# Kernel tuning notes

Measured on AMD Instinct MI355X. Metric: run time of the kernel, lower is better.

## Reference

```python
import jax, jax.numpy as jnp
import numpy as np

N_HEADS = 4


def _mha(q, k, v, in_w, in_b, out_w, out_b):
    # torch nn.MultiheadAttention (batch_first). q: [..., Lq, C], k/v: [..., Lk, C].
    # Leading batch dims broadcast (used for the factorized per-slice attention).
    C = q.shape[-1]
    dh = C // N_HEADS
    wq, wk, wv = jnp.split(in_w, 3, axis=0)
    bq, bk, bv = jnp.split(in_b, 3, axis=0)
    qh = (q @ wq.T + bq).reshape(q.shape[:-1] + (N_HEADS, dh))
    kh = (k @ wk.T + bk).reshape(k.shape[:-1] + (N_HEADS, dh))
    vh = (v @ wv.T + bv).reshape(v.shape[:-1] + (N_HEADS, dh))
    logits = jnp.einsum('...qhd,...khd->...hqk', qh, kh) / np.sqrt(dh).astype(np.float32)
    alpha = jax.nn.softmax(logits, axis=-1)
    o = jnp.einsum('...hqk,...khd->...qhd', alpha, vh)
    o = o.reshape(o.shape[:-2] + (C,))
    return o @ out_w.T + out_b


def _layernorm(x, w, b):
    m = x.mean(-1, keepdims=True)
    v = x.var(-1, keepdims=True)
    return (x - m) * jax.lax.rsqrt(v + 1e-5) * w + b


def reference(h, hist0, hist1, dw_w, pw_w, gn_w, gn_b, gr1_scale, gr1_gw, gr1_gb,
              global_tokens, mha_in_w, mha_in_b, mha_out_w, mha_out_b,
              ln_w, ln_b, gr2_scale, gr2_gw, gr2_gb, rms_w, blk_w, Hx, Hy, Hz):
    B, N, C = h.shape
    M = global_tokens.shape[0]

    # ---------------- DepthwiseConv3d block ----------------
    # 'b (hz hy hx) c -> b c hx hy hz'
    h3 = h.reshape(B, Hz, Hy, Hx, C).transpose(0, 4, 3, 2, 1)  # [B,C,Hx,Hy,Hz]
    y = jax.lax.conv_general_dilated(
        h3, dw_w, window_strides=(1, 1, 1), padding=((1, 1), (1, 1), (1, 1)),
        dimension_numbers=('NCDHW', 'OIDHW', 'NCDHW'), feature_group_count=C)
    # GroupNorm(num_groups=min(32,C))
    G = min(32, C)
    yg = y.reshape(B, G, C // G, Hx, Hy, Hz)
    mu = yg.mean(axis=(2, 3, 4, 5), keepdims=True)
    var = yg.var(axis=(2, 3, 4, 5), keepdims=True)
    y = ((yg - mu) * jax.lax.rsqrt(var + 1e-5)).reshape(B, C, Hx, Hy, Hz)
    y = y * gn_w[None, :, None, None, None] + gn_b[None, :, None, None, None]
    y = jax.nn.gelu(y, approximate=False)  # torch nn.GELU default = exact erf
    y = jnp.einsum('bcxyz,oc->boxyz', y, pw_w)  # 1x1x1 pointwise conv
    delta = y.transpose(0, 4, 3, 2, 1).reshape(B, N, C)  # back to 'b (hz hy hx) c'
    h = h + gr1_scale * jax.nn.sigmoid(h @ gr1_gw.T + gr1_gb) * delta

    # ---------------- FactorizedCrossAttn ----------------
    h_xyz = h.reshape(B, Hz, Hy, Hx, C).transpose(0, 3, 2, 1, 4)  # [B,Hx,Hy,Hz,C]
    Q = jnp.broadcast_to(global_tokens, (B, M, C))
    Qb = Q[:, None]  # [B,1,M,C]; broadcasts over slices instead of materializing expand

    kv_x = h_xyz.transpose(0, 2, 3, 1, 4).reshape(B, Hy * Hz, Hx, C)
    tok_x = _mha(Qb, kv_x, kv_x, mha_in_w[0], mha_in_b[0], mha_out_w[0], mha_out_b[0]).mean(1)
    kv_y = h_xyz.transpose(0, 1, 3, 2, 4).reshape(B, Hx * Hz, Hy, C)
    tok_y = _mha(Qb, kv_y, kv_y, mha_in_w[1], mha_in_b[1], mha_out_w[1], mha_out_b[1]).mean(1)
    kv_z = h_xyz.reshape(B, Hx * Hy, Hz, C)
    tok_z = _mha(Qb, kv_z, kv_z, mha_in_w[2], mha_in_b[2], mha_out_w[2], mha_out_b[2]).mean(1)

    tokens = tok_x + tok_y + tok_z
    t_in = _layernorm(tokens, ln_w[0], ln_b[0])
    tokens = _mha(t_in, t_in, t_in, mha_in_w[3], mha_in_b[3], mha_out_w[3], mha_out_b[3])
    h_normed = _layernorm(h, ln_w[1], ln_b[1])
    glob = _mha(h_normed, tokens, tokens, mha_in_w[4], mha_in_b[4], mha_out_w[4], mha_out_b[4])
    h = h + gr2_scale * jax.nn.sigmoid(h @ gr2_gw.T + gr2_gb) * glob

    # ---------------- block_attn_res ----------------
    V = jnp.stack([hist0, hist1, h], axis=0)  # [S,B,N,C], S=3
    K = V * jax.lax.rsqrt(jnp.mean(V * V, axis=-1, keepdims=True) + 1e-6) * rms_w  # RMSNorm
    logits = jnp.clip(jnp.einsum('d,sbnd->sbn', blk_w, K), -30.0, 30.0)
    alpha = jax.nn.softmax(logits, axis=0)
    return jnp.einsum('sbn,sbnd->bnd', alpha, V)


def setup_inputs() -> dict:
    key = jax.random.key(0)
    ks = jax.random.split(key, 16)
    B, C, Hx, Hy, Hz, M = 2, 128, 64, 64, 32, 64
    N = Hx * Hy * Hz

    def g(k, shape, scale):
        return jax.random.normal(k, shape, dtype=jnp.float32) * scale

    return {
        'h': g(ks[0], (B, N, C), 1.0),
        'hist0': g(ks[1], (B, N, C), 1.0),
        'hist1': g(ks[2], (B, N, C), 1.0),
        'dw_w': g(ks[3], (C, 1, 3, 3, 3), 0.27),  # kaiming_normal_ fan_in=27
        'pw_w': jnp.ones((C, C), jnp.float32) / C,  # code uses ones_; scaled for stability
        'gn_w': jnp.ones((C,), jnp.float32),
        'gn_b': jnp.zeros((C,), jnp.float32),
        'gr1_scale': jnp.float32(0.01),
        'gr1_gw': g(ks[4], (C, C), 0.02),
        'gr1_gb': jnp.zeros((C,), jnp.float32),
        'global_tokens': g(ks[5], (M, C), 0.09),  # xavier_uniform-ish scale
        'mha_in_w': g(ks[6], (5, 3 * C, C), 0.06),
        'mha_in_b': jnp.zeros((5, 3 * C), jnp.float32),
        'mha_out_w': g(ks[7], (5, C, C), 0.06),
        'mha_out_b': jnp.zeros((5, C), jnp.float32),
        'ln_w': jnp.ones((2, C), jnp.float32),
        'ln_b': jnp.zeros((2, C), jnp.float32),
        'gr2_scale': jnp.float32(0.01),
        'gr2_gw': g(ks[8], (C, C), 0.02),
        'gr2_gb': jnp.zeros((C,), jnp.float32),
        'rms_w': jnp.ones((C,), jnp.float32),
        'blk_w': g(ks[9], (C,), 0.09),
        'Hx': Hx, 'Hy': Hy, 'Hz': Hz,
    }
```

## Files before the change

kernel.cpp:

```cpp
#include <hip/hip_runtime.h>
#include <hip/hip_bf16.h>

#define B_ 2
#define C_ 128
#define HX_ 64
#define HY_ 64
#define HZ_ 32
#define N_ 131072
#define M_ 64
#define G_ 32
#define SCALE_ 0.17677669529663687f

typedef unsigned short u16;
typedef __bf16 bf16x8 __attribute__((ext_vector_type(8)));
typedef float f32x4 __attribute__((ext_vector_type(4)));

#define MFMA(a, b, c) __builtin_amdgcn_mfma_f32_16x16x32_bf16(a, b, c, 0, 0, 0)

__device__ __forceinline__ float bf2f(u16 u){
    return __uint_as_float(((unsigned int)u) << 16);
}
__device__ __forceinline__ u16 f2bf(float f){
    unsigned int u = __float_as_uint(f);
    unsigned int r = (u + 0x7FFFu + ((u >> 16) & 1u)) >> 16;
    return (u16)r;
}
__device__ __forceinline__ bf16x8 ldf(const u16* p){
    return __builtin_bit_cast(bf16x8, *reinterpret_cast<const uint4*>(p));
}
__device__ __forceinline__ float wred_sum(float v){
    for (int o = 32; o; o >>= 1) v += __shfl_xor(v, o);
    return v;
}

__global__ __launch_bounds__(256) void k_wcvt(const float* __restrict__ pw, const float* __restrict__ g1w,
        const float* __restrict__ in_w, const float* __restrict__ out_w, const float* __restrict__ g2w,
        u16* __restrict__ wA, u16* __restrict__ wKV, u16* __restrict__ wQ, u16* __restrict__ wO, u16* __restrict__ wG2){
    int idx = blockIdx.x*256 + threadIdx.x;
    if (idx < 32768){
        int j = idx >> 7, k = idx & 127;
        wA[idx] = f2bf(j < 128 ? pw[j*128 + k] : g1w[(j-128)*128 + k]);
    } else if (idx < 131072){
        int r = idx - 32768;
        int a = r >> 15, jk = r & 32767;
        int j = jk >> 7, k = jk & 127;
        wKV[r] = f2bf(in_w[((size_t)a*384 + 128 + j)*128 + k]);
    } else if (idx < 147456){
        int r = idx - 131072;
        wQ[r] = f2bf(in_w[4*384*128 + r]);
    } else if (idx < 163840){
        int r = idx - 147456;
        wO[r] = f2bf(out_w[4*128*128 + r]);
    } else if (idx < 180224){
        int r = idx - 163840;
        wG2[r] = f2bf(g2w[r]);
    }
}

__global__ __launch_bounds__(256, 2) void k_conv3(const float* __restrict__ h,
        const float* __restrict__ dw_w, u16* __restrict__ ybf, u16* __restrict__ hb16,
        float* __restrict__ gstats){
    int t = threadIdx.x;
    int lane = t & 31;
    int c4 = lane << 2;
    int xg = t >> 5;
    int bi = blockIdx.x;
    int b = bi >> 9;
    int y = (bi >> 3) & 63;
    int x = ((bi & 7) << 3) | xg;
    const float* hb = h + (size_t)b*N_*C_;
    u16* yb = ybf + (size_t)b*N_*C_;
    u16* hbb = hb16 + (size_t)b*N_*C_;
    f32x4 wv[27];
    int off[9];
    #pragma unroll
    for (int dxi = 0; dxi < 3; ++dxi){
        #pragma unroll
        for (int dyi = 0; dyi < 3; ++dyi){
            int xr = x + dxi - 1, yr = y + dyi - 1;
            float m = (xr >= 0 && xr < HX_ && yr >= 0 && yr < HY_) ? 1.f : 0.f;
            int xx = min(max(xr, 0), HX_-1);
            int yy = min(max(yr, 0), HY_-1);
            off[dxi*3+dyi] = (yy*64 + xx)*128 + c4;
            #pragma unroll
            for (int dzi = 0; dzi < 3; ++dzi){
                int k = (dxi*3+dyi)*3+dzi;
                int wk = dxi*9 + dyi*3 + dzi;
                f32x4 wq;
                #pragma unroll
                for (int e = 0; e < 4; ++e) wq[e] = dw_w[(c4+e)*27 + wk] * m;
                wv[k] = wq;
            }
        }
    }
    f32x4 accA = {0,0,0,0}, accB = {0,0,0,0}, accC = {0,0,0,0};
    f32x4 sum4 = {0,0,0,0}, ss4 = {0,0,0,0};
    #pragma unroll 2
    for (int zp = 0; zp < 32; ++zp){
        size_t zb = (size_t)zp*524288;
        f32x4 v[9];
        #pragma unroll
        for (int j = 0; j < 9; ++j) v[j] = *(const f32x4*)(hb + zb + off[j]);
        {
            unsigned int p0 = (unsigned int)f2bf(v[4][0]) | ((unsigned int)f2bf(v[4][1]) << 16);
            unsigned int p1 = (unsigned int)f2bf(v[4][2]) | ((unsigned int)f2bf(v[4][3]) << 16);
            uint2 pk = {p0, p1};
            *(uint2*)(hbb + zb + off[4]) = pk;
        }
        f32x4 s0 = {0,0,0,0}, s1 = {0,0,0,0}, s2 = {0,0,0,0};
        #pragma unroll
        for (int j = 0; j < 9; ++j){
            s0 += v[j]*wv[j*3+0];
            s1 += v[j]*wv[j*3+1];
            s2 += v[j]*wv[j*3+2];
        }
        accA += s2; accB += s1; accC += s0;
        if (zp >= 1){
            f32x4 yv = accA;
            sum4 += yv; ss4 += yv*yv;
            unsigned int p0 = (unsigned int)f2bf(yv[0]) | ((unsigned int)f2bf(yv[1]) << 16);
            unsigned int p1 = (unsigned int)f2bf(yv[2]) | ((unsigned int)f2bf(yv[3]) << 16);
            uint2 pk = {p0, p1};
            *(uint2*)(yb + (size_t)(zp-1)*524288 + off[4]) = pk;
        }
        accA = accB; accB = accC; accC = (f32x4){0,0,0,0};
    }
    {
        f32x4 yv = accA;
        sum4 += yv; ss4 += yv*yv;
        unsigned int p0 = (unsigned int)f2bf(yv[0]) | ((unsigned int)f2bf(yv[1]) << 16);
        unsigned int p1 = (unsigned int)f2bf(yv[2]) | ((unsigned int)f2bf(yv[3]) << 16);
        uint2 pk = {p0, p1};
        *(uint2*)(yb + (size_t)31*524288 + off[4]) = pk;
    }
    float sum = sum4[0]+sum4[1]+sum4[2]+sum4[3];
    float ss  = ss4[0]+ss4[1]+ss4[2]+ss4[3];
    sum += __shfl_xor(sum, 32);
    ss  += __shfl_xor(ss, 32);
    if ((t & 32) == 0){
        atomicAdd(&gstats[(b*G_ + lane)*2 + 0], sum);
        atomicAdd(&gstats[(b*G_ + lane)*2 + 1], ss);
    }
}

__global__ void k_gstats_fin(const float* __restrict__ gstats, float* __restrict__ gfin){
    int t = threadIdx.x;
    if (t < B_*G_){
        const float cnt = 4.f * (float)N_;
        float mean = gstats[t*2] / cnt;
        float var  = gstats[t*2+1] / cnt - mean*mean;
        gfin[t*2]   = mean;
        gfin[t*2+1] = rsqrtf(var + 1e-5f);
    }
}

__global__ __launch_bounds__(256) void k_stageA(const u16* __restrict__ ybf, const u16* __restrict__ hb16,
        const float* __restrict__ gfin, const float* __restrict__ gn_w, const float* __restrict__ gn_b,
        const float* __restrict__ g1b, const float* __restrict__ s1p,
        const u16* __restrict__ wA, u16* __restrict__ h1b){
    __shared__ __align__(16) u16 sU[64*136];
    __shared__ __align__(16) u16 sH[64*136];
    __shared__ float sPar[384];
    int t = threadIdx.x;
    int w = t >> 6, l = t & 63, lm = l & 15, kq = l >> 4;
    if (t < 128){ sPar[t] = gn_w[t]; sPar[128+t] = gn_b[t]; sPar[256+t] = gfin[t]; }
    bf16x8 wUf[2][4], wGf[2][4];
    float gbias[2];
    #pragma unroll
    for (int jt = 0; jt < 2; ++jt){
        int j = w*32 + jt*16 + lm;
        gbias[jt] = g1b[j];
        #pragma unroll
        for (int ks = 0; ks < 4; ++ks){
            wUf[jt][ks] = ldf(wA + (size_t)j*128 + ks*32 + kq*8);
            wGf[jt][ks] = ldf(wA + (size_t)(128+j)*128 + ks*32 + kq*8);
        }
    }
    float s1 = s1p[0];
    __syncthreads();
    for (int it = 0; it < 4; ++it){
        int tile = blockIdx.x + it*1024;
        size_t r0 = (size_t)tile*64;
        int bsel = (tile >= 2048) ? 1 : 0;
        for (int pass = 0; pass < 4; ++pass){
            int cid = pass*256 + t;
            int row = cid >> 4, col8 = (cid & 15)*8;
            size_t gi = (r0 + row)*C_ + col8;
            uint4 yraw = *(const uint4*)(ybf + gi);
            uint4 hraw = *(const uint4*)(hb16 + gi);
            const u16* yp = (const u16*)&yraw;
            unsigned int pu[4];
            #pragma unroll
            for (int p2 = 0; p2 < 4; ++p2){
                u16 r2[2];
                #pragma unroll
                for (int e2 = 0; e2 < 2; ++e2){
                    int e = p2*2 + e2;
                    int ch = col8 + e;
                    int g = ch >> 2;
                    float mean = sPar[256 + (bsel*32+g)*2];
                    float inv  = sPar[256 + (bsel*32+g)*2 + 1];
                    float v = (bf2f(yp[e]) - mean)*inv*sPar[ch] + sPar[128+ch];
                    float u = 0.5f*v*(1.f + erff(v*0.70710678118654752f));
                    r2[e2] = f2bf(u);
                }
                pu[p2] = (unsigned int)r2[0] | ((unsigned int)r2[1] << 16);
            }
            *(uint4*)(sU + row*136 + col8) = *(uint4*)pu;
            *(uint4*)(sH + row*136 + col8) = hraw;
        }
        __syncthreads();
        f32x4 accU[4][2], accG[4][2];
        #pragma unroll
        for (int rt = 0; rt < 4; ++rt)
            #pragma unroll
            for (int jt = 0; jt < 2; ++jt){
                accU[rt][jt] = (f32x4){0.f,0.f,0.f,0.f};
                accG[rt][jt] = (f32x4){gbias[jt],gbias[jt],gbias[jt],gbias[jt]};
            }
        #pragma unroll
        for (int rt = 0; rt < 4; ++rt)
            #pragma unroll
            for (int ks = 0; ks < 4; ++ks){
                bf16x8 aU = ldf(sU + (rt*16+lm)*136 + ks*32 + kq*8);
                bf16x8 aH = ldf(sH + (rt*16+lm)*136 + ks*32 + kq*8);
                #pragma unroll
                for (int jt = 0; jt < 2; ++jt){
                    accU[rt][jt] = MFMA(aU, wUf[jt][ks], accU[rt][jt]);
                    accG[rt][jt] = MFMA(aH, wGf[jt][ks], accG[rt][jt]);
                }
            }
        #pragma unroll
        for (int rt = 0; rt < 4; ++rt)
            #pragma unroll
            for (int jt = 0; jt < 2; ++jt){
                int col = w*32 + jt*16 + lm;
                #pragma unroll
                for (int r = 0; r < 4; ++r){
                    int lrow = rt*16 + kq*4 + r;
                    float g = 1.f/(1.f + expf(-accG[rt][jt][r]));
                    float hv = bf2f(sH[lrow*136 + col]);
                    float h1v = hv + s1*g*accU[rt][jt][r];
                    h1b[(r0 + lrow)*C_ + col] = f2bf(h1v);
                }
            }
        __syncthreads();
    }
}

__global__ __launch_bounds__(256) void k_qh_axes(const float* __restrict__ gtok,
        const float* __restrict__ in_w, const float* __restrict__ in_b, float* __restrict__ qhT){
    int idx = blockIdx.x*256 + threadIdx.x;
    int m = idx & 63;
    int hd = (idx >> 6) & 127;
    int a = idx >> 13;
    float acc = in_b[a*384 + hd];
    const float* w = in_w + ((size_t)a*384 + hd)*C_;
    const float* q = gtok + (size_t)m*C_;
    for (int c = 0; c < C_; ++c) acc += q[c]*w[c];
    qhT[idx] = acc;
}

template<int AXIS, int L, int S>
__global__ __launch_bounds__(256, 2) void k_axis_attn(const u16* __restrict__ h1b,
        const u16* __restrict__ wKVb, const float* __restrict__ in_b,
        const float* __restrict__ qhT, float* __restrict__ o_mean){
    constexpr int SLICES = 8;
    constexpr int PARTS = S / SLICES;
    constexpr int PSROW = L + 8;
    constexpr int PSZ = 64 * PSROW;
    constexpr int NT = L / 16;
    constexpr int KS = L / 32;
    __shared__ __align__(16) u16 sm[6*PSZ];
    int t = threadIdx.x;
    int w = t >> 6, l = t & 63, lm = l & 15, kq = l >> 4;
    int b = blockIdx.x / PARTS;
    int part = blockIdx.x % PARTS;
    u16* rows = sm;
    u16* kv   = sm + 2*PSZ;
    u16* vT   = sm + 4*PSZ;
    u16* Ps   = sm + w*PSZ;
    bf16x8 wf[4][4];
    float bias[4];
    #pragma unroll
    for (int jt = 0; jt < 4; ++jt){
        int j = w*64 + jt*16 + lm;
        bias[jt] = in_b[AXIS*384 + 128 + j];
        #pragma unroll
        for (int ks = 0; ks < 4; ++ks)
            wf[jt][ks] = ldf(wKVb + ((size_t)AXIS*256 + j)*128 + ks*32 + kq*8);
    }
    bf16x8 qf[4];
    #pragma unroll
    for (int mt = 0; mt < 4; ++mt){
        union { u16 u[8]; bf16x8 v; } tmp;
        #pragma unroll
        for (int e = 0; e < 8; ++e)
            tmp.u[e] = f2bf(qhT[(AXIS*C_ + w*32 + kq*8 + e)*64 + mt*16 + lm] * SCALE_);
        qf[mt] = tmp.v;
    }
    f32x4 oacc[4][2];
    #pragma unroll
    for (int mt = 0; mt < 4; ++mt)
        #pragma unroll
        for (int dt = 0; dt < 2; ++dt)
            oacc[mt][dt] = (f32x4){0.f,0.f,0.f,0.f};
    const u16* hb = h1b + (size_t)b*N_*C_;
    for (int si = 0; si < SLICES; ++si){
        int s = part*SLICES + si;
        for (int ci = t; ci < L*16; ci += 256){
            int p = ci >> 4, c8 = (ci & 15)*8;
            int n;
            if (AXIS == 0){ int yy = s >> 5, zz = s & 31; n = zz*4096 + yy*64 + p; }
            else if (AXIS == 1){ int xx = s >> 5, zz = s & 31; n = zz*4096 + p*64 + xx; }
            else { int xx = s >> 6, yy = s & 63; n = p*4096 + yy*64 + xx; }
            *(uint4*)(rows + p*136 + c8) = *(const uint4*)(hb + (size_t)n*C_ + c8);
        }
        __syncthreads();
        #pragma unroll
        for (int rt = 0; rt < NT; ++rt){
            f32x4 acc[4];
            #pragma unroll
            for (int jt = 0; jt < 4; ++jt) acc[jt] = (f32x4){bias[jt],bias[jt],bias[jt],bias[jt]};
            #pragma unroll
            for (int ks = 0; ks < 4; ++ks){
                bf16x8 a = ldf(rows + (rt*16+lm)*136 + ks*32 + kq*8);
                #pragma unroll
                for (int jt = 0; jt < 4; ++jt) acc[jt] = MFMA(a, wf[jt][ks], acc[jt]);
            }
            #pragma unroll
            for (int jt = 0; jt < 4; ++jt){
                int j = w*64 + jt*16 + lm;
                #pragma unroll
                for (int r = 0; r < 4; ++r){
                    int key = rt*16 + kq*4 + r;
                    if (w < 2) kv[key*136 + j] = f2bf(acc[jt][r]);
                    else       vT[(j-128)*PSROW + key] = f2bf(acc[jt][r]);
                }
            }
        }
        __syncthreads();
        f32x4 lacc[4][NT];
        #pragma unroll
        for (int mt = 0; mt < 4; ++mt)
            #pragma unroll
            for (int nt = 0; nt < NT; ++nt) lacc[mt][nt] = (f32x4){0.f,0.f,0.f,0.f};
        #pragma unroll
        for (int nt = 0; nt < NT; ++nt){
            bf16x8 kf = ldf(kv + (nt*16+lm)*136 + w*32 + kq*8);
            #pragma unroll
            for (int mt = 0; mt < 4; ++mt) lacc[mt][nt] = MFMA(qf[mt], kf, lacc[mt][nt]);
        }
        __syncthreads();
        #pragma unroll
        for (int mt = 0; mt < 4; ++mt){
            #pragma unroll
            for (int r = 0; r < 4; ++r){
                float mx = lacc[mt][0][r];
                #pragma unroll
                for (int nt = 1; nt < NT; ++nt) mx = fmaxf(mx, lacc[mt][nt][r]);
                mx = fmaxf(mx, __shfl_xor(mx,1));
                mx = fmaxf(mx, __shfl_xor(mx,2));
                mx = fmaxf(mx, __shfl_xor(mx,4));
                mx = fmaxf(mx, __shfl_xor(mx,8));
                float ev[NT]; float sum = 0.f;
                #pragma unroll
                for (int nt = 0; nt < NT; ++nt){ ev[nt] = expf(lacc[mt][nt][r] - mx); sum += ev[nt]; }
                sum += __shfl_xor(sum,1);
                sum += __shfl_xor(sum,2);
                sum += __shfl_xor(sum,4);
                sum += __shfl_xor(sum,8);
                float inv = 1.f/sum;
                #pragma unroll
                for (int nt = 0; nt < NT; ++nt)
                    Ps[(mt*16 + kq*4 + r)*PSROW + nt*16 + lm] = f2bf(ev[nt]*inv);
            }
        }
        #pragma unroll
        for (int ks = 0; ks < KS; ++ks){
            bf16x8 vb[2];
            #pragma unroll
            for (int dt = 0; dt < 2; ++dt)
                vb[dt] = ldf(vT + (w*32 + dt*16 + lm)*PSROW + ks*32 + kq*8);
            #pragma unroll
            for (int mt = 0; mt < 4; ++mt){
                bf16x8 pa = ldf(Ps + (mt*16+lm)*PSROW + ks*32 + kq*8);
                #pragma unroll
                for (int dt = 0; dt < 2; ++dt)
                    oacc[mt][dt] = MFMA(pa, vb[dt], oacc[mt][dt]);
            }
        }
        __syncthreads();
    }
    const float invS = 1.f / (float)S;
    float* om = o_mean + (size_t)(AXIS*B_ + b)*M_*C_;
    #pragma unroll
    for (int mt = 0; mt < 4; ++mt)
        #pragma unroll
        for (int dt = 0; dt < 2; ++dt)
            #pragma unroll
            for (int r = 0; r < 4; ++r){
                int m = mt*16 + kq*4 + r;
                int d = dt*16 + lm;
                atomicAdd(&om[m*C_ + w*32 + d], oacc[mt][dt][r]*invS);
            }
}

__global__ __launch_bounds__(256) void k_tokens(const float* __restrict__ o_mean,
        const float* __restrict__ out_w, const float* __restrict__ out_b, float* __restrict__ tokens){
    int idx = blockIdx.x*256 + threadIdx.x;
    int c = idx & 127;
    int m = (idx >> 7) & 63;
    int b = idx >> 13;
    float acc = 0.f;
    for (int a = 0; a < 3; ++a){
        const float* om = o_mean + ((size_t)(a*B_ + b)*M_ + m)*C_;
        const float* w = out_w + ((size_t)a*C_ + c)*C_;
        float s = out_b[a*C_ + c];
        for (int k = 0; k < C_; ++k) s += om[k]*w[k];
        acc += s;
    }
    tokens[idx] = acc;
}

__global__ __launch_bounds__(128) void k_ln(const float* __restrict__ in,
        const float* __restrict__ w, const float* __restrict__ b, float* __restrict__ out){
    int r = blockIdx.x;
    int c = threadIdx.x;
    float v = in[(size_t)r*C_ + c];
    __shared__ float red[4];
    float s = wred_sum(v), ss = wred_sum(v*v);
    int wv = c >> 6;
    if ((c & 63) == 0){ red[wv*2] = s; red[wv*2+1] = ss; }
    __syncthreads();
    float S = red[0] + red[2], SS = red[1] + red[3];
    float mean = S / 128.f;
    float var = SS / 128.f - mean*mean;
    out[(size_t)r*C_ + c] = (v - mean) * rsqrtf(var + 1e-5f) * w[c] + b[c];
}

__global__ __launch_bounds__(256) void k_qkv3(const float* __restrict__ t_in,
        const float* __restrict__ in_w, const float* __restrict__ in_b, float* __restrict__ qkv3){
    int idx = blockIdx.x*256 + threadIdx.x;
    int j = idx % 384;
    int m = (idx / 384) & 63;
    int b = idx / (384*64);
    const float* x = t_in + ((size_t)b*64 + m)*C_;
    const float* w = in_w + ((size_t)3*384 + j)*C_;
    float acc = in_b[3*384 + j];
    for (int c = 0; c < C_; ++c) acc += x[c]*w[c];
    qkv3[idx] = acc;
}

__global__ __launch_bounds__(64) void k_attn3(const float* __restrict__ qkv3, float* __restrict__ o3){
    int b = blockIdx.x >> 2, hh = blockIdx.x & 3;
    int m = threadIdx.x;
    const float* base = qkv3 + (size_t)b*64*384;
    float q[32];
    #pragma unroll
    for (int d = 0; d < 32; ++d) q[d] = base[m*384 + hh*32 + d];
    float lg[64]; float mx = -1e30f;
    for (int mk = 0; mk < 64; ++mk){
        float acc = 0.f;
        #pragma unroll
        for (int d = 0; d < 32; ++d) acc += q[d] * base[mk*384 + 128 + hh*32 + d];
        acc *= SCALE_;
        lg[mk] = acc; mx = fmaxf(mx, acc);
    }
    float sum = 0.f;
    #pragma unroll
    for (int mk = 0; mk < 64; ++mk){ float e = expf(lg[mk]-mx); lg[mk] = e; sum += e; }
    float inv = 1.f/sum;
    float o[32];
    #pragma unroll
    for (int d = 0; d < 32; ++d) o[d] = 0.f;
    for (int mk = 0; mk < 64; ++mk){
        float al = lg[mk]*inv;
        #pragma unroll
        for (int d = 0; d < 32; ++d) o[d] += al * base[mk*384 + 256 + hh*32 + d];
    }
    #pragma unroll
    for (int d = 0; d < 32; ++d) o3[((size_t)b*64 + m)*C_ + hh*32 + d] = o[d];
}

__global__ __launch_bounds__(256) void k_tokens2(const float* __restrict__ o3,
        const float* __restrict__ out_w, const float* __restrict__ out_b, float* __restrict__ tokens2){
    int idx = blockIdx.x*256 + threadIdx.x;
    int c = idx & 127;
    int m = (idx >> 7) & 63;
    int b = idx >> 13;
    const float* x = o3 + ((size_t)b*64 + m)*C_;
    const float* w = out_w + ((size_t)3*C_ + c)*C_;
    float acc = out_b[3*C_ + c];
    for (int k = 0; k < C_; ++k) acc += x[k]*w[k];
    tokens2[idx] = acc;
}

__global__ __launch_bounds__(256) void k_kv4(const float* __restrict__ tokens2,
        const float* __restrict__ in_w, const float* __restrict__ in_b,
        u16* __restrict__ khs, u16* __restrict__ vhb){
    int idx = blockIdx.x*256 + threadIdx.x;
    int b = idx >> 14;
    int r = idx & 16383;
    if (r < 8192){
        int hh = r >> 11, key = (r >> 5) & 63, d = r & 31;
        int hd = hh*32 + d;
        const float* x = tokens2 + ((size_t)b*64 + key)*C_;
        const float* w = in_w + ((size_t)4*384 + 128 + hd)*C_;
        float acc = in_b[4*384 + 128 + hd];
        for (int c = 0; c < C_; ++c) acc += x[c]*w[c];
        khs[(size_t)b*8192 + r] = f2bf(acc * SCALE_);
    } else {
        int rr = r - 8192;
        int key = rr >> 7, c = rr & 127;
        const float* x = tokens2 + ((size_t)b*64 + key)*C_;
        const float* w = in_w + ((size_t)4*384 + 256 + c)*C_;
        float acc = in_b[4*384 + 256 + c];
        for (int k = 0; k < 128; ++k) acc += x[k]*w[k];
        vhb[(size_t)b*8192 + rr] = f2bf(acc);
    }
}

__global__ __launch_bounds__(256) void k_globfinal(const u16* __restrict__ h1b,
        const u16* __restrict__ wQb, const u16* __restrict__ wOb, const u16* __restrict__ wG2b,
        const u16* __restrict__ khs, const u16* __restrict__ vhb,
        const float* __restrict__ in_b, const float* __restrict__ out_b,
        const float* __restrict__ g2b, const float* __restrict__ s2p,
        const float* __restrict__ ln_w, const float* __restrict__ ln_b,
        const float* __restrict__ hist0, const float* __restrict__ hist1,
        const float* __restrict__ rms_w, const float* __restrict__ blk_w,
        float* __restrict__ outp){
    __shared__ __align__(16) u16 sm[22016];
    __shared__ float sLn[384];
    int t = threadIdx.x;
    int w = t >> 6, l = t & 63, lm = l & 15, kq = l >> 4;
    if (t < 128){ sLn[t] = ln_w[128+t]; sLn[128+t] = ln_b[128+t]; sLn[256+t] = blk_w[t]*rms_w[t]; }
    int b = blockIdx.x >> 9;
    bf16x8 wQf[2][4], wOf[2][4], wGf[2][4], khf[4], vf[2][2];
    float qb[2], ob[2], gb[2];
    #pragma unroll
    for (int jt = 0; jt < 2; ++jt){
        int j = w*32 + jt*16 + lm;
        qb[jt] = in_b[4*384 + j];
        ob[jt] = out_b[4*128 + j];
        gb[jt] = g2b[j];
        #pragma unroll
        for (int ks = 0; ks < 4; ++ks){
            wQf[jt][ks] = ldf(wQb + (size_t)j*128 + ks*32 + kq*8);
            wOf[jt][ks] = ldf(wOb + (size_t)j*128 + ks*32 + kq*8);
            wGf[jt][ks] = ldf(wG2b + (size_t)j*128 + ks*32 + kq*8);
        }
    }
    #pragma unroll
    for (int jt = 0; jt < 4; ++jt)
        khf[jt] = ldf(khs + ((size_t)(b*4 + w)*64 + jt*16 + lm)*32 + kq*8);
    #pragma unroll
    for (int jt = 0; jt < 2; ++jt)
        #pragma unroll
        for (int ks = 0; ks < 2; ++ks){
            union { u16 u[8]; bf16x8 v; } tmp;
            #pragma unroll
            for (int e = 0; e < 8; ++e){
                int key = ks*32 + kq*8 + e;
                tmp.u[e] = vhb[(size_t)(b*64 + key)*128 + w*32 + jt*16 + lm];
            }
            vf[jt][ks] = tmp.v;
        }
    float s2 = s2p[0];
    __syncthreads();

    for (int it = 0; it < 4; ++it){
        int tile = (blockIdx.x & 511) + it*512;
        size_t r0 = (size_t)b*N_ + (size_t)tile*64;
        {
            int r = t >> 2, q = t & 3;
            const u16* src = h1b + (r0 + r)*C_ + q*32;
            uint4 raw[4];
            float v[32];
            float s = 0.f, ss = 0.f;
            #pragma unroll
            for (int c4 = 0; c4 < 4; ++c4){
                raw[c4] = *(const uint4*)(src + c4*8);
                const u16* pu = (const u16*)&raw[c4];
                #pragma unroll
                for (int e = 0; e < 8; ++e){ float x = bf2f(pu[e]); v[c4*8+e] = x; s += x; ss += x*x; }
            }
            s += __shfl_xor(s,1); s += __shfl_xor(s,2);
            ss += __shfl_xor(ss,1); ss += __shfl_xor(ss,2);
            float mean = s*(1.f/128.f);
            float inv = rsqrtf(ss*(1.f/128.f) - mean*mean + 1e-5f);
            #pragma unroll
            for (int c4 = 0; c4 < 4; ++c4){
                unsigned int o[4];
                #pragma unroll
                for (int p2 = 0; p2 < 4; ++p2){
                    int c = q*32 + c4*8 + p2*2;
                    u16 a0 = f2bf((v[c4*8+p2*2]   - mean)*inv*sLn[c]   + sLn[128+c]);
                    u16 a1 = f2bf((v[c4*8+p2*2+1] - mean)*inv*sLn[c+1] + sLn[128+c+1]);
                    o[p2] = (unsigned int)a0 | ((unsigned int)a1 << 16);
                }
                *(uint4*)(sm + 0    + r*136 + q*32 + c4*8) = *(uint4*)o;
                *(uint4*)(sm + 8704 + r*136 + q*32 + c4*8) = raw[c4];
            }
        }
        __syncthreads();
        f32x4 accQ[4][2];
        #pragma unroll
        for (int rt = 0; rt < 4; ++rt)
            #pragma unroll
            for (int jt = 0; jt < 2; ++jt)
                accQ[rt][jt] = (f32x4){qb[jt],qb[jt],qb[jt],qb[jt]};
        #pragma unroll
        for (int rt = 0; rt < 4; ++rt)
            #pragma unroll
            for (int ks = 0; ks < 4; ++ks){
                bf16x8 a = ldf(sm + 0 + (rt*16+lm)*136 + ks*32 + kq*8);
                #pragma unroll
                for (int jt = 0; jt < 2; ++jt)
                    accQ[rt][jt] = MFMA(a, wQf[jt][ks], accQ[rt][jt]);
            }
        __syncthreads();
        #pragma unroll
        for (int rt = 0; rt < 4; ++rt)
            #pragma unroll
            for (int jt = 0; jt < 2; ++jt)
                #pragma unroll
                for (int r = 0; r < 4; ++r)
                    sm[0 + (rt*16+kq*4+r)*136 + w*32+jt*16+lm] = f2bf(accQ[rt][jt][r]);
        u16* Ps = sm + 17408 + w*1152;
        #pragma unroll
        for (int mt = 0; mt < 4; ++mt){
            bf16x8 aq = ldf(sm + 0 + (mt*16+lm)*136 + w*32 + kq*8);
            f32x4 lacc[4];
            #pragma unroll
            for (int jt = 0; jt < 4; ++jt) lacc[jt] = (f32x4){0.f,0.f,0.f,0.f};
            #pragma unroll
            for (int jt = 0; jt < 4; ++jt) lacc[jt] = MFMA(aq, khf[jt], lacc[jt]);
            #pragma unroll
            for (int r = 0; r < 4; ++r){
                float v0 = lacc[0][r], v1 = lacc[1][r], v2 = lacc[2][r], v3 = lacc[3][r];
                float mx = fmaxf(fmaxf(v0,v1), fmaxf(v2,v3));
                mx = fmaxf(mx, __shfl_xor(mx,1));
                mx = fmaxf(mx, __shfl_xor(mx,2));
                mx = fmaxf(mx, __shfl_xor(mx,4));
                mx = fmaxf(mx, __shfl_xor(mx,8));
                float e0 = expf(v0-mx), e1 = expf(v1-mx), e2 = expf(v2-mx), e3 = expf(v3-mx);
                float sum = e0+e1+e2+e3;
                sum += __shfl_xor(sum,1);
                sum += __shfl_xor(sum,2);
                sum += __shfl_xor(sum,4);
                sum += __shfl_xor(sum,8);
                float inv = 1.f/sum;
                Ps[(kq*4+r)*72 + lm     ] = f2bf(e0*inv);
                Ps[(kq*4+r)*72 + lm + 16] = f2bf(e1*inv);
                Ps[(kq*4+r)*72 + lm + 32] = f2bf(e2*inv);
                Ps[(kq*4+r)*72 + lm + 48] = f2bf(e3*inv);
            }
            f32x4 of[2];
            #pragma unroll
            for (int jt = 0; jt < 2; ++jt) of[jt] = (f32x4){0.f,0.f,0.f,0.f};
            #pragma unroll
            for (int ks = 0; ks < 2; ++ks){
                bf16x8 ap = ldf(Ps + lm*72 + ks*32 + kq*8);
                #pragma unroll
                for (int jt = 0; jt < 2; ++jt)
                    of[jt] = MFMA(ap, vf[jt][ks], of[jt]);
            }
            #pragma unroll
            for (int jt = 0; jt < 2; ++jt)
                #pragma unroll
                for (int r = 0; r < 4; ++r)
                    sm[0 + (mt*16+kq*4+r)*136 + w*32+jt*16+lm] = f2bf(of[jt][r]);
        }
        __syncthreads();
        f32x4 accO[4][2], accG[4][2];
        #pragma unroll
        for (int rt = 0; rt < 4; ++rt)
            #pragma unroll
            for (int jt = 0; jt < 2; ++jt){
                accO[rt][jt] = (f32x4){ob[jt],ob[jt],ob[jt],ob[jt]};
                accG[rt][jt] = (f32x4){gb[jt],gb[jt],gb[jt],gb[jt]};
            }
        #pragma unroll
        for (int rt = 0; rt < 4; ++rt)
            #pragma unroll
            for (int ks = 0; ks < 4; ++ks){
                bf16x8 ao = ldf(sm + 0    + (rt*16+lm)*136 + ks*32 + kq*8);
                bf16x8 ah = ldf(sm + 8704 + (rt*16+lm)*136 + ks*32 + kq*8);
                #pragma unroll
                for (int jt = 0; jt < 2; ++jt){
                    accO[rt][jt] = MFMA(ao, wOf[jt][ks], accO[rt][jt]);
                    accG[rt][jt] = MFMA(ah, wGf[jt][ks], accG[rt][jt]);
                }
            }
        #pragma unroll
        for (int rt = 0; rt < 4; ++rt)
            #pragma unroll
            for (int jt = 0; jt < 2; ++jt){
                int col = w*32 + jt*16 + lm;
                #pragma unroll
                for (int r = 0; r < 4; ++r){
                    int lrow = rt*16 + kq*4 + r;
                    float hv = bf2f(sm[8704 + lrow*136 + col]);
                    float g = 1.f/(1.f + expf(-accG[rt][jt][r]));
                    accO[rt][jt][r] = hv + s2*g*accO[rt][jt][r];
                }
            }
        __syncthreads();
        #pragma unroll
        for (int rt = 0; rt < 4; ++rt)
            #pragma unroll
            for (int jt = 0; jt < 2; ++jt){
                int col = w*32 + jt*16 + lm;
                #pragma unroll
                for (int r = 0; r < 4; ++r)
                    sm[8704 + (rt*16+kq*4+r)*132 + col] = f2bf(accO[rt][jt][r]);
            }
        __syncthreads();
        {
            int r = t >> 2, q = t & 3;
            size_t row = r0 + r;
            const u16* h2p = sm + 8704 + r*132 + q*32;
            float h2a[32], v0a[32], v1a[32];
            float ss0 = 0.f, ss1 = 0.f, ss2 = 0.f, q0 = 0.f, q1 = 0.f, q2 = 0.f;
            #pragma unroll
            for (int c4 = 0; c4 < 8; ++c4){
                uint2 hk = *(const uint2*)(h2p + c4*4);
                float4 a0 = *(const float4*)(hist0 + row*C_ + q*32 + c4*4);
                float4 a1 = *(const float4*)(hist1 + row*C_ + q*32 + c4*4);
                const u16* pu = (const u16*)&hk;
                const float* p0 = (const float*)&a0;
                const float* p1 = (const float*)&a1;
                #pragma unroll
                for (int e = 0; e < 4; ++e){
                    float bw = sLn[256 + q*32 + c4*4 + e];
                    float x2 = bf2f(pu[e]), x0 = p0[e], x1 = p1[e];
                    h2a[c4*4+e] = x2; v0a[c4*4+e] = x0; v1a[c4*4+e] = x1;
                    ss0 += x0*x0; ss1 += x1*x1; ss2 += x2*x2;
                    q0 += bw*x0; q1 += bw*x1; q2 += bw*x2;
                }
            }
            ss0 += __shfl_xor(ss0,1); ss0 += __shfl_xor(ss0,2);
            ss1 += __shfl_xor(ss1,1); ss1 += __shfl_xor(ss1,2);
            ss2 += __shfl_xor(ss2,1); ss2 += __shfl_xor(ss2,2);
            q0 += __shfl_xor(q0,1); q0 += __shfl_xor(q0,2);
            q1 += __shfl_xor(q1,1); q1 += __shfl_xor(q1,2);
            q2 += __shfl_xor(q2,1); q2 += __shfl_xor(q2,2);
            float i0 = rsqrtf(ss0*(1.f/128.f) + 1e-6f);
            float i1 = rsqrtf(ss1*(1.f/128.f) + 1e-6f);
            float i2 = rsqrtf(ss2*(1.f/128.f) + 1e-6f);
            float l0 = fminf(fmaxf(q0*i0, -30.f), 30.f);
            float l1 = fminf(fmaxf(q1*i1, -30.f), 30.f);
            float l2 = fminf(fmaxf(q2*i2, -30.f), 30.f);
            float mx = fmaxf(l0, fmaxf(l1, l2));
            float e0 = expf(l0-mx), e1 = expf(l1-mx), e2 = expf(l2-mx);
            float isum = 1.f/(e0+e1+e2);
            #pragma unroll
            for (int c4 = 0; c4 < 8; ++c4){
                float o[4];
                #pragma unroll
                for (int e = 0; e < 4; ++e){
                    int i = c4*4+e;
                    o[e] = (e0*v0a[i] + e1*v1a[i] + e2*h2a[i])*isum;
                }
                *(float4*)(outp + row*C_ + q*32 + c4*4) = *(float4*)o;
            }
        }
        __syncthreads();
    }
}

extern "C" void kernel_launch(void* const* d_in, const int* in_sizes, int n_in,
                              void* d_out, int out_size, void* d_ws, size_t ws_size,
                              hipStream_t stream){
    (void)in_sizes; (void)n_in; (void)out_size; (void)ws_size;
    const float* h     = (const float*)d_in[0];
    const float* hist0 = (const float*)d_in[1];
    const float* hist1 = (const float*)d_in[2];
    const float* dw_w  = (const float*)d_in[3];
    const float* pw_w  = (const float*)d_in[4];
    const float* gn_w  = (const float*)d_in[5];
    const float* gn_b  = (const float*)d_in[6];
    const float* gr1_s = (const float*)d_in[7];
    const float* gr1_gw= (const float*)d_in[8];
    const float* gr1_gb= (const float*)d_in[9];
    const float* gtok  = (const float*)d_in[10];
    const float* in_w  = (const float*)d_in[11];
    const float* in_b  = (const float*)d_in[12];
    const float* out_w = (const float*)d_in[13];
    const float* out_b = (const float*)d_in[14];
    const float* ln_w  = (const float*)d_in[15];
    const float* ln_b  = (const float*)d_in[16];
    const float* gr2_s = (const float*)d_in[17];
    const float* gr2_gw= (const float*)d_in[18];
    const float* gr2_gb= (const float*)d_in[19];
    const float* rms_w = (const float*)d_in[20];
    const float* blk_w = (const float*)d_in[21];
    float* out = (float*)d_out;

    u16* ybf  = (u16*)d_out;
    u16* hb16 = (u16*)d_out + (size_t)B_*N_*C_;

    float* W = (float*)d_ws;
    size_t off = 0;
    float* gstats  = W + off; off += 128;
    float* gfin    = W + off; off += 128;
    float* qhT     = W + off; off += 3*128*64;
    float* o_mean  = W + off; off += 3*B_*M_*C_;
    float* tokens  = W + off; off += B_*M_*C_;
    float* t_in    = W + off; off += B_*M_*C_;
    float* qkv3    = W + off; off += B_*M_*384;
    float* o3      = W + off; off += B_*M_*C_;
    float* tokens2 = W + off; off += B_*M_*C_;
    u16* U = (u16*)(W + off);
    size_t uo = 0;
    u16* h1b = U + uo; uo += (size_t)B_*N_*C_;
    u16* wA  = U + uo; uo += 256*128;
    u16* wKV = U + uo; uo += 3*256*128;
    u16* wQ  = U + uo; uo += 128*128;
    u16* wO  = U + uo; uo += 128*128;
    u16* wG2 = U + uo; uo += 128*128;
    u16* khs = U + uo; uo += B_*4*64*32;
    u16* vhb = U + uo; uo += B_*64*128;

    hipMemsetAsync(gstats, 0, 128*sizeof(float), stream);
    hipMemsetAsync(o_mean, 0, 3*B_*M_*C_*sizeof(float), stream);
    k_wcvt<<<704, 256, 0, stream>>>(pw_w, gr1_gw, in_w, out_w, gr2_gw, wA, wKV, wQ, wO, wG2);
    k_conv3<<<1024, 256, 0, stream>>>(h, dw_w, ybf, hb16, gstats);
    k_gstats_fin<<<1, 64, 0, stream>>>(gstats, gfin);
    k_stageA<<<1024, 256, 0, stream>>>(ybf, hb16, gfin, gn_w, gn_b, gr1_gb, gr1_s, wA, h1b);
    k_qh_axes<<<96, 256, 0, stream>>>(gtok, in_w, in_b, qhT);
    k_axis_attn<0,64,2048><<<512, 256, 0, stream>>>(h1b, wKV, in_b, qhT, o_mean);
    k_axis_attn<1,64,2048><<<512, 256, 0, stream>>>(h1b, wKV, in_b, qhT, o_mean);
    k_axis_attn<2,32,4096><<<1024, 256, 0, stream>>>(h1b, wKV, in_b, qhT, o_mean);
    k_tokens<<<64, 256, 0, stream>>>(o_mean, out_w, out_b, tokens);
    k_ln<<<B_*M_, 128, 0, stream>>>(tokens, ln_w, ln_b, t_in);
    k_qkv3<<<192, 256, 0, stream>>>(t_in, in_w, in_b, qkv3);
    k_attn3<<<8, 64, 0, stream>>>(qkv3, o3);
    k_tokens2<<<64, 256, 0, stream>>>(o3, out_w, out_b, tokens2);
    k_kv4<<<128, 256, 0, stream>>>(tokens2, in_w, in_b, khs, vhb);
    k_globfinal<<<1024, 256, 0, stream>>>(h1b, wQ, wO, wG2, khs, vhb, in_b, out_b,
                                          gr2_gb, gr2_s, ln_w, ln_b, hist0, hist1, rms_w, blk_w, out);
}
```

Baseline: 1.092 ms.

## Split global-attention final kernel into one-tile-per-block attention and separate history-mix kernel

The fused persistent final kernel, which held all weight fragments in registers and looped over four tiles, is split in two. The attention, gating and residual step now runs one 64-row tile per block with weights loaded per k-step and launch bounds asking for four blocks per SM, and writes h2 as bf16 to a new workspace buffer. A second grid-stride kernel reads h2, hist0 and hist1 to do the RMS-gated three-way mix. The aim is to cut register pressure and raise occupancy, at the cost of an extra round trip of h2 through global memory and repeated weight loads per tile.

```diff
diff --git a/kernel.cpp b/kernel.cpp
--- a/kernel.cpp
+++ b/kernel.cpp
@@ -521,112 +521,102 @@
     }
 }
 
-__global__ __launch_bounds__(256) void k_globfinal(const u16* __restrict__ h1b,
+__global__ __launch_bounds__(256, 4) void k_glob2(const u16* __restrict__ h1b,
         const u16* __restrict__ wQb, const u16* __restrict__ wOb, const u16* __restrict__ wG2b,
         const u16* __restrict__ khs, const u16* __restrict__ vhb,
         const float* __restrict__ in_b, const float* __restrict__ out_b,
         const float* __restrict__ g2b, const float* __restrict__ s2p,
         const float* __restrict__ ln_w, const float* __restrict__ ln_b,
-        const float* __restrict__ hist0, const float* __restrict__ hist1,
-        const float* __restrict__ rms_w, const float* __restrict__ blk_w,
-        float* __restrict__ outp){
+        u16* __restrict__ h2b){
     __shared__ __align__(16) u16 sm[22016];
-    __shared__ float sLn[384];
+    __shared__ float sLn[256];
     int t = threadIdx.x;
     int w = t >> 6, l = t & 63, lm = l & 15, kq = l >> 4;
-    if (t < 128){ sLn[t] = ln_w[128+t]; sLn[128+t] = ln_b[128+t]; sLn[256+t] = blk_w[t]*rms_w[t]; }
-    int b = blockIdx.x >> 9;
-    bf16x8 wQf[2][4], wOf[2][4], wGf[2][4], khf[4], vf[2][2];
-    float qb[2], ob[2], gb[2];
-    #pragma unroll
-    for (int jt = 0; jt < 2; ++jt){
-        int j = w*32 + jt*16 + lm;
-        qb[jt] = in_b[4*384 + j];
-        ob[jt] = out_b[4*128 + j];
-        gb[jt] = g2b[j];
-        #pragma unroll
-        for (int ks = 0; ks < 4; ++ks){
-            wQf[jt][ks] = ldf(wQb + (size_t)j*128 + ks*32 + kq*8);
-            wOf[jt][ks] = ldf(wOb + (size_t)j*128 + ks*32 + kq*8);
-            wGf[jt][ks] = ldf(wG2b + (size_t)j*128 + ks*32 + kq*8);
-        }
-    }
-    #pragma unroll
-    for (int jt = 0; jt < 4; ++jt)
-        khf[jt] = ldf(khs + ((size_t)(b*4 + w)*64 + jt*16 + lm)*32 + kq*8);
-    #pragma unroll
-    for (int jt = 0; jt < 2; ++jt)
-        #pragma unroll
-        for (int ks = 0; ks < 2; ++ks){
-            union { u16 u[8]; bf16x8 v; } tmp;
-            #pragma unroll
-            for (int e = 0; e < 8; ++e){
-                int key = ks*32 + kq*8 + e;
-                tmp.u[e] = vhb[(size_t)(b*64 + key)*128 + w*32 + jt*16 + lm];
-            }
-            vf[jt][ks] = tmp.v;
-        }
+    if (t < 128){ sLn[t] = ln_w[128+t]; sLn[128+t] = ln_b[128+t]; }
+    int tile = blockIdx.x;
+    int b = tile >> 11;
+    size_t r0 = (size_t)tile * 64;
+    int j0 = w*32 + lm, j1 = w*32 + 16 + lm;
     float s2 = s2p[0];
     __syncthreads();
-
-    for (int it = 0; it < 4; ++it){
-        int tile = (blockIdx.x & 511) + it*512;
-        size_t r0 = (size_t)b*N_ + (size_t)tile*64;
-        {
-            int r = t >> 2, q = t & 3;
-            const u16* src = h1b + (r0 + r)*C_ + q*32;
-            uint4 raw[4];
-            float v[32];
-            float s = 0.f, ss = 0.f;
-            #pragma unroll
-            for (int c4 = 0; c4 < 4; ++c4){
-                raw[c4] = *(const uint4*)(src + c4*8);
-                const u16* pu = (const u16*)&raw[c4];
-                #pragma unroll
-                for (int e = 0; e < 8; ++e){ float x = bf2f(pu[e]); v[c4*8+e] = x; s += x; ss += x*x; }
-            }
-            s += __shfl_xor(s,1); s += __shfl_xor(s,2);
-            ss += __shfl_xor(ss,1); ss += __shfl_xor(ss,2);
-            float mean = s*(1.f/128.f);
-            float inv = rsqrtf(ss*(1.f/128.f) - mean*mean + 1e-5f);
-            #pragma unroll
-            for (int c4 = 0; c4 < 4; ++c4){
-                unsigned int o[4];
-                #pragma unroll
-                for (int p2 = 0; p2 < 4; ++p2){
-                    int c = q*32 + c4*8 + p2*2;
-                    u16 a0 = f2bf((v[c4*8+p2*2]   - mean)*inv*sLn[c]   + sLn[128+c]);
-                    u16 a1 = f2bf((v[c4*8+p2*2+1] - mean)*inv*sLn[c+1] + sLn[128+c+1]);
-                    o[p2] = (unsigned int)a0 | ((unsigned int)a1 << 16);
+    {
+        int r = t >> 2, q = t & 3;
+        const u16* src = h1b + (r0 + r)*C_ + q*32;
+        uint4 raw[4];
+        float v[32];
+        float s = 0.f, ss = 0.f;
+        #pragma unroll
+        for (int c4 = 0; c4 < 4; ++c4){
+            raw[c4] = *(const uint4*)(src + c4*8);
+            const u16* pu = (const u16*)&raw[c4];
+            #pragma unroll
+            for (int e = 0; e < 8; ++e){ float x = bf2f(pu[e]); v[c4*8+e] = x; s += x; ss += x*x; }
+        }
+        s += __shfl_xor(s,1); s += __shfl_xor(s,2);
+        ss += __shfl_xor(ss,1); ss += __shfl_xor(ss,2);
+        float mean = s*(1.f/128.f);
+        float inv = rsqrtf(ss*(1.f/128.f) - mean*mean + 1e-5f);
+        #pragma unroll
+        for (int c4 = 0; c4 < 4; ++c4){
+            unsigned int o[4];
+            #pragma unroll
+            for (int p2 = 0; p2 < 4; ++p2){
+                int c = q*32 + c4*8 + p2*2;
+                u16 a0 = f2bf((v[c4*8+p2*2]   - mean)*inv*sLn[c]   + sLn[128+c]);
+                u16 a1 = f2bf((v[c4*8+p2*2+1] - mean)*inv*sLn[c+1] + sLn[128+c+1]);
+                o[p2] = (unsigned int)a0 | ((unsigned int)a1 << 16);
+            }
+            *(uint4*)(sm + 0    + r*136 + q*32 + c4*8) = *(uint4*)o;
+            *(uint4*)(sm + 8704 + r*136 + q*32 + c4*8) = raw[c4];
+        }
+    }
+    __syncthreads();
+    f32x4 accQ[4][2];
+    {
+        float qb0 = in_b[4*384 + j0], qb1 = in_b[4*384 + j1];
+        #pragma unroll
+        for (int rt = 0; rt < 4; ++rt){
+            accQ[rt][0] = (f32x4){qb0,qb0,qb0,qb0};
+            accQ[rt][1] = (f32x4){qb1,qb1,qb1,qb1};
+        }
+    }
+    #pragma unroll
+    for (int ks = 0; ks < 4; ++ks){
+        bf16x8 wq0 = ldf(wQb + (size_t)j0*128 + ks*32 + kq*8);
+        bf16x8 wq1 = ldf(wQb + (size_t)j1*128 + ks*32 + kq*8);
+        #pragma unroll
+        for (int rt = 0; rt < 4; ++rt){
+            bf16x8 a = ldf(sm + 0 + (rt*16+lm)*136 + ks*32 + kq*8);
+            accQ[rt][0] = MFMA(a, wq0, accQ[rt][0]);
+            accQ[rt][1] = MFMA(a, wq1, accQ[rt][1]);
+        }
+    }
+    __syncthreads();
+    #pragma unroll
+    for (int rt = 0; rt < 4; ++rt)
+        #pragma unroll
+        for (int jt = 0; jt < 2; ++jt)
+            #pragma unroll
+            for (int r = 0; r < 4; ++r)
+                sm[0 + (rt*16+kq*4+r)*136 + w*32+jt*16+lm] = f2bf(accQ[rt][jt][r]);
+    {
+        bf16x8 khf[4];
+        #pragma unroll
+        for (int jt = 0; jt < 4; ++jt)
+            khf[jt] = ldf(khs + ((size_t)(b*4 + w)*64 + jt*16 + lm)*32 + kq*8);
+        bf16x8 vf[2][2];
+        #pragma unroll
+        for (int jt = 0; jt < 2; ++jt)
+            #pragma unroll
+            for (int ks = 0; ks < 2; ++ks){
+                union { u16 u[8]; bf16x8 v; } tmp;
+                #pragma unroll
+                for (int e = 0; e < 8; ++e){
+                    int key = ks*32 + kq*8 + e;
+                    tmp.u[e] = vhb[(size_t)(b*64 + key)*128 + w*32 + jt*16 + lm];
                 }
-                *(uint4*)(sm + 0    + r*136 + q*32 + c4*8) = *(uint4*)o;
-                *(uint4*)(sm + 8704 + r*136 + q*32 + c4*8) = raw[c4];
-            }
-        }
-        __syncthreads();
-        f32x4 accQ[4][2];
-        #pragma unroll
-        for (int rt = 0; rt < 4; ++rt)
-            #pragma unroll
-            for (int jt = 0; jt < 2; ++jt)
-                accQ[rt][jt] = (f32x4){qb[jt],qb[jt],qb[jt],qb[jt]};
-        #pragma unroll
-        for (int rt = 0; rt < 4; ++rt)
-            #pragma unroll
-            for (int ks = 0; ks < 4; ++ks){
-                bf16x8 a = ldf(sm + 0 + (rt*16+lm)*136 + ks*32 + kq*8);
-                #pragma unroll
-                for (int jt = 0; jt < 2; ++jt)
-                    accQ[rt][jt] = MFMA(a, wQf[jt][ks], accQ[rt][jt]);
-            }
-        __syncthreads();
-        #pragma unroll
-        for (int rt = 0; rt < 4; ++rt)
-            #pragma unroll
-            for (int jt = 0; jt < 2; ++jt)
-                #pragma unroll
-                for (int r = 0; r < 4; ++r)
-                    sm[0 + (rt*16+kq*4+r)*136 + w*32+jt*16+lm] = f2bf(accQ[rt][jt][r]);
+                vf[jt][ks] = tmp.v;
+            }
         u16* Ps = sm + 17408 + w*1152;
         #pragma unroll
         for (int mt = 0; mt < 4; ++mt){
@@ -672,101 +662,133 @@
                 for (int r = 0; r < 4; ++r)
                     sm[0 + (mt*16+kq*4+r)*136 + w*32+jt*16+lm] = f2bf(of[jt][r]);
         }
-        __syncthreads();
-        f32x4 accO[4][2], accG[4][2];
-        #pragma unroll
-        for (int rt = 0; rt < 4; ++rt)
-            #pragma unroll
-            for (int jt = 0; jt < 2; ++jt){
-                accO[rt][jt] = (f32x4){ob[jt],ob[jt],ob[jt],ob[jt]};
-                accG[rt][jt] = (f32x4){gb[jt],gb[jt],gb[jt],gb[jt]};
-            }
-        #pragma unroll
-        for (int rt = 0; rt < 4; ++rt)
-            #pragma unroll
-            for (int ks = 0; ks < 4; ++ks){
-                bf16x8 ao = ldf(sm + 0    + (rt*16+lm)*136 + ks*32 + kq*8);
-                bf16x8 ah = ldf(sm + 8704 + (rt*16+lm)*136 + ks*32 + kq*8);
-                #pragma unroll
-                for (int jt = 0; jt < 2; ++jt){
-                    accO[rt][jt] = MFMA(ao, wOf[jt][ks], accO[rt][jt]);
-                    accG[rt][jt] = MFMA(ah, wGf[jt][ks], accG[rt][jt]);
-                }
-            }
-        #pragma unroll
-        for (int rt = 0; rt < 4; ++rt)
-            #pragma unroll
-            for (int jt = 0; jt < 2; ++jt){
-                int col = w*32 + jt*16 + lm;
-                #pragma unroll
-                for (int r = 0; r < 4; ++r){
-                    int lrow = rt*16 + kq*4 + r;
-                    float hv = bf2f(sm[8704 + lrow*136 + col]);
-                    float g = 1.f/(1.f + expf(-accG[rt][jt][r]));
-                    accO[rt][jt][r] = hv + s2*g*accO[rt][jt][r];
-                }
-            }
-        __syncthreads();
-        #pragma unroll
-        for (int rt = 0; rt < 4; ++rt)
-            #pragma unroll
-            for (int jt = 0; jt < 2; ++jt){
-                int col = w*32 + jt*16 + lm;
-                #pragma unroll
-                for (int r = 0; r < 4; ++r)
-                    sm[8704 + (rt*16+kq*4+r)*132 + col] = f2bf(accO[rt][jt][r]);
-            }
-        __syncthreads();
-        {
-            int r = t >> 2, q = t & 3;
-            size_t row = r0 + r;
-            const u16* h2p = sm + 8704 + r*132 + q*32;
-            float h2a[32], v0a[32], v1a[32];
-            float ss0 = 0.f, ss1 = 0.f, ss2 = 0.f, q0 = 0.f, q1 = 0.f, q2 = 0.f;
-            #pragma unroll
-            for (int c4 = 0; c4 < 8; ++c4){
-                uint2 hk = *(const uint2*)(h2p + c4*4);
-                float4 a0 = *(const float4*)(hist0 + row*C_ + q*32 + c4*4);
-                float4 a1 = *(const float4*)(hist1 + row*C_ + q*32 + c4*4);
-                const u16* pu = (const u16*)&hk;
-                const float* p0 = (const float*)&a0;
-                const float* p1 = (const float*)&a1;
-                #pragma unroll
-                for (int e = 0; e < 4; ++e){
-                    float bw = sLn[256 + q*32 + c4*4 + e];
-                    float x2 = bf2f(pu[e]), x0 = p0[e], x1 = p1[e];
-                    h2a[c4*4+e] = x2; v0a[c4*4+e] = x0; v1a[c4*4+e] = x1;
-                    ss0 += x0*x0; ss1 += x1*x1; ss2 += x2*x2;
-                    q0 += bw*x0; q1 += bw*x1; q2 += bw*x2;
-                }
-            }
-            ss0 += __shfl_xor(ss0,1); ss0 += __shfl_xor(ss0,2);
-            ss1 += __shfl_xor(ss1,1); ss1 += __shfl_xor(ss1,2);
-            ss2 += __shfl_xor(ss2,1); ss2 += __shfl_xor(ss2,2);
-            q0 += __shfl_xor(q0,1); q0 += __shfl_xor(q0,2);
-            q1 += __shfl_xor(q1,1); q1 += __shfl_xor(q1,2);
-            q2 += __shfl_xor(q2,1); q2 += __shfl_xor(q2,2);
-            float i0 = rsqrtf(ss0*(1.f/128.f) + 1e-6f);
-            float i1 = rsqrtf(ss1*(1.f/128.f) + 1e-6f);
-            float i2 = rsqrtf(ss2*(1.f/128.f) + 1e-6f);
-            float l0 = fminf(fmaxf(q0*i0, -30.f), 30.f);
-            float l1 = fminf(fmaxf(q1*i1, -30.f), 30.f);
-            float l2 = fminf(fmaxf(q2*i2, -30.f), 30.f);
-            float mx = fmaxf(l0, fmaxf(l1, l2));
-            float e0 = expf(l0-mx), e1 = expf(l1-mx), e2 = expf(l2-mx);
-            float isum = 1.f/(e0+e1+e2);
-            #pragma unroll
-            for (int c4 = 0; c4 < 8; ++c4){
-                float o[4];
-                #pragma unroll
-                for (int e = 0; e < 4; ++e){
-                    int i = c4*4+e;
-                    o[e] = (e0*v0a[i] + e1*v1a[i] + e2*h2a[i])*isum;
-                }
-                *(float4*)(outp + row*C_ + q*32 + c4*4) = *(float4*)o;
-            }
-        }
-        __syncthreads();
+    }
+    __syncthreads();
+    f32x4 accO[4][2], accG[4][2];
+    {
+        float ob0 = out_b[4*128 + j0], ob1 = out_b[4*128 + j1];
+        float gb0 = g2b[j0], gb1 = g2b[j1];
+        #pragma unroll
+        for (int rt = 0; rt < 4; ++rt){
+            accO[rt][0] = (f32x4){ob0,ob0,ob0,ob0};
+            accO[rt][1] = (f32x4){ob1,ob1,ob1,ob1};
+            accG[rt][0] = (f32x4){gb0,gb0,gb0,gb0};
+            accG[rt][1] = (f32x4){gb1,gb1,gb1,gb1};
+        }
+    }
+    #pragma unroll
+    for (int ks = 0; ks < 4; ++ks){
+        bf16x8 wo0 = ldf(wOb  + (size_t)j0*128 + ks*32 + kq*8);
+        bf16x8 wo1 = ldf(wOb  + (size_t)j1*128 + ks*32 + kq*8);
+        bf16x8 wg0 = ldf(wG2b + (size_t)j0*128 + ks*32 + kq*8);
+        bf16x8 wg1 = ldf(wG2b + (size_t)j1*128 + ks*32 + kq*8);
+        #pragma unroll
+        for (int rt = 0; rt < 4; ++rt){
+            bf16x8 ao = ldf(sm + 0    + (rt*16+lm)*136 + ks*32 + kq*8);
+            bf16x8 ah = ldf(sm + 8704 + (rt*16+lm)*136 + ks*32 + kq*8);
+            accO[rt][0] = MFMA(ao, wo0, accO[rt][0]);
+            accO[rt][1] = MFMA(ao, wo1, accO[rt][1]);
+            accG[rt][0] = MFMA(ah, wg0, accG[rt][0]);
+            accG[rt][1] = MFMA(ah, wg1, accG[rt][1]);
+        }
+    }
+    #pragma unroll
+    for (int rt = 0; rt < 4; ++rt)
+        #pragma unroll
+        for (int jt = 0; jt < 2; ++jt){
+            int col = w*32 + jt*16 + lm;
+            #pragma unroll
+            for (int r = 0; r < 4; ++r){
+                int lrow = rt*16 + kq*4 + r;
+                float hv = bf2f(sm[8704 + lrow*136 + col]);
+                float g = 1.f/(1.f + expf(-accG[rt][jt][r]));
+                accO[rt][jt][r] = hv + s2*g*accO[rt][jt][r];
+            }
+        }
+    __syncthreads();
+    #pragma unroll
+    for (int rt = 0; rt < 4; ++rt)
+        #pragma unroll
+        for (int jt = 0; jt < 2; ++jt){
+            int col = w*32 + jt*16 + lm;
+            #pragma unroll
+            for (int r = 0; r < 4; ++r)
+                sm[8704 + (rt*16+kq*4+r)*136 + col] = f2bf(accO[rt][jt][r]);
+        }
+    __syncthreads();
+    {
+        int r = t >> 2, q = t & 3;
+        u16* dst = h2b + (r0 + r)*C_ + q*32;
+        #pragma unroll
+        for (int c4 = 0; c4 < 4; ++c4)
+            *(uint4*)(dst + c4*8) = *(const uint4*)(sm + 8704 + r*136 + q*32 + c4*8);
+    }
+}
+
+__global__ __launch_bounds__(256) void k_final2(const u16* __restrict__ h2b,
+        const float* __restrict__ hist0, const float* __restrict__ hist1,
+        const float* __restrict__ rms_w, const float* __restrict__ blk_w,
+        float* __restrict__ outp){
+    __shared__ float sbw[128];
+    int t = threadIdx.x;
+    if (t < 128) sbw[t] = blk_w[t]*rms_w[t];
+    __syncthreads();
+    const int TOT = B_*N_*4;
+    for (int idx = blockIdx.x*256 + t; idx < TOT; idx += gridDim.x*256){
+        int r = idx >> 2, q = idx & 3;
+        size_t row = r;
+        const u16* h2p = h2b + row*C_ + q*32;
+        float h2a[32], v0a[32], v1a[32];
+        float ss0 = 0.f, ss1 = 0.f, ss2 = 0.f, q0 = 0.f, q1 = 0.f, q2 = 0.f;
+        #pragma unroll
+        for (int c4 = 0; c4 < 4; ++c4){
+            uint4 hk = *(const uint4*)(h2p + c4*8);
+            float4 a0 = *(const float4*)(hist0 + row*C_ + q*32 + c4*8);
+            float4 a0b = *(const float4*)(hist0 + row*C_ + q*32 + c4*8 + 4);
+            float4 a1 = *(const float4*)(hist1 + row*C_ + q*32 + c4*8);
+            float4 a1b = *(const float4*)(hist1 + row*C_ + q*32 + c4*8 + 4);
+            const u16* pu = (const u16*)&hk;
+            const float* p0 = (const float*)&a0;
+            const float* p0b = (const float*)&a0b;
+            const float* p1 = (const float*)&a1;
+            const float* p1b = (const float*)&a1b;
+            #pragma unroll
+            for (int e = 0; e < 8; ++e){
+                int i = c4*8 + e;
+                float bw = sbw[q*32 + i];
+                float x2 = bf2f(pu[e]);
+                float x0 = (e < 4) ? p0[e] : p0b[e-4];
+                float x1 = (e < 4) ? p1[e] : p1b[e-4];
+                h2a[i] = x2; v0a[i] = x0; v1a[i] = x1;
+                ss0 += x0*x0; ss1 += x1*x1; ss2 += x2*x2;
+                q0 += bw*x0; q1 += bw*x1; q2 += bw*x2;
+            }
+        }
+        ss0 += __shfl_xor(ss0,1); ss0 += __shfl_xor(ss0,2);
+        ss1 += __shfl_xor(ss1,1); ss1 += __shfl_xor(ss1,2);
+        ss2 += __shfl_xor(ss2,1); ss2 += __shfl_xor(ss2,2);
+        q0 += __shfl_xor(q0,1); q0 += __shfl_xor(q0,2);
+        q1 += __shfl_xor(q1,1); q1 += __shfl_xor(q1,2);
+        q2 += __shfl_xor(q2,1); q2 += __shfl_xor(q2,2);
+        float i0 = rsqrtf(ss0*(1.f/128.f) + 1e-6f);
+        float i1 = rsqrtf(ss1*(1.f/128.f) + 1e-6f);
+        float i2 = rsqrtf(ss2*(1.f/128.f) + 1e-6f);
+        float l0 = fminf(fmaxf(q0*i0, -30.f), 30.f);
+        float l1 = fminf(fmaxf(q1*i1, -30.f), 30.f);
+        float l2 = fminf(fmaxf(q2*i2, -30.f), 30.f);
+        float mx = fmaxf(l0, fmaxf(l1, l2));
+        float e0 = expf(l0-mx), e1 = expf(l1-mx), e2 = expf(l2-mx);
+        float isum = 1.f/(e0+e1+e2);
+        #pragma unroll
+        for (int c4 = 0; c4 < 8; ++c4){
+            float o[4];
+            #pragma unroll
+            for (int e = 0; e < 4; ++e){
+                int i = c4*4+e;
+                o[e] = (e0*v0a[i] + e1*v1a[i] + e2*h2a[i])*isum;
+            }
+            *(float4*)(outp + row*C_ + q*32 + c4*4) = *(float4*)o;
+        }
     }
 }
 
@@ -815,6 +837,7 @@
     u16* U = (u16*)(W + off);
     size_t uo = 0;
     u16* h1b = U + uo; uo += (size_t)B_*N_*C_;
+    u16* h2b = U + uo; uo += (size_t)B_*N_*C_;
     u16* wA  = U + uo; uo += 256*128;
     u16* wKV = U + uo; uo += 3*256*128;
     u16* wQ  = U + uo; uo += 128*128;
@@ -839,6 +862,7 @@
     k_attn3<<<8, 64, 0, stream>>>(qkv3, o3);
     k_tokens2<<<64, 256, 0, stream>>>(o3, out_w, out_b, tokens2);
     k_kv4<<<128, 256, 0, stream>>>(tokens2, in_w, in_b, khs, vhb);
-    k_globfinal<<<1024, 256, 0, stream>>>(h1b, wQ, wO, wG2, khs, vhb, in_b, out_b,
-                                          gr2_gb, gr2_s, ln_w, ln_b, hist0, hist1, rms_w, blk_w, out);
-}
+    k_glob2<<<4096, 256, 0, stream>>>(h1b, wQ, wO, wG2, khs, vhb, in_b, out_b,
+                                      gr2_gb, gr2_s, ln_w, ln_b, h2b);
+    k_final2<<<2048, 256, 0, stream>>>(h2b, hist0, hist1, rms_w, blk_w, out);
+}
```

After: 1.037 ms, median of 3. -5.0%, faster.
